# Optimization experiments

Measured on AMD Instinct MI355X. Metric: run time of the kernel, lower is better.

The kernel has to match this reference:

```python
import jax, jax.numpy as jnp
import numpy as np

D_MODEL = 1024
N_HEADS = 16
D_K = D_MODEL // N_HEADS
SEQ = 4096
BATCH = 1
THETA = 10000.0


def setup_inputs() -> dict:
    key = jax.random.key(0)
    ks = jax.random.split(key, 5)
    scale = 0.02
    x = jax.random.normal(ks[0], (BATCH, SEQ, D_MODEL), dtype=jnp.float32)
    token_positions = jnp.broadcast_to(jnp.arange(SEQ, dtype=jnp.int64 if jax.config.jax_enable_x64 else jnp.int32)[None, :], (BATCH, SEQ))
    Wq = jax.random.normal(ks[1], (D_MODEL, D_MODEL), dtype=jnp.float32) * scale
    Wk = jax.random.normal(ks[2], (D_MODEL, D_MODEL), dtype=jnp.float32) * scale
    Wv = jax.random.normal(ks[3], (D_MODEL, D_MODEL), dtype=jnp.float32) * scale
    Wo = jax.random.normal(ks[4], (D_MODEL, D_MODEL), dtype=jnp.float32) * scale
    return {"x": x, "token_positions": token_positions, "Wq": Wq, "Wk": Wk, "Wv": Wv, "Wo": Wo}


def _apply_rope(t, token_positions, theta=THETA):
    # t: (b, h, s, d_k); token_positions: (b, s)
    d_k = t.shape[-1]
    inv_freq = theta ** (-jnp.arange(0, d_k, 2, dtype=jnp.float32) / d_k)  # (d_k/2,)
    ang = token_positions.astype(jnp.float32)[:, :, None] * inv_freq  # (b, s, d_k/2)
    cos = jnp.cos(ang)[:, None, :, :]  # (b, 1, s, d_k/2)
    sin = jnp.sin(ang)[:, None, :, :]
    te, to = t[..., 0::2], t[..., 1::2]
    re = te * cos - to * sin
    ro = te * sin + to * cos
    # interleave back: (..., d_k/2, 2) -> (..., d_k)
    return jnp.stack([re, ro], axis=-1).reshape(t.shape)


def reference(x, token_positions, Wq, Wk, Wv, Wo):
    b, s, d_model = x.shape
    h, d_k = N_HEADS, D_K
    q = (x @ Wq.T).reshape(b, s, h, d_k).transpose(0, 2, 1, 3)  # (b,h,s,d_k)
    k = (x @ Wk.T).reshape(b, s, h, d_k).transpose(0, 2, 1, 3)
    v = (x @ Wv.T).reshape(b, s, h, d_k).transpose(0, 2, 1, 3)
    q = _apply_rope(q, token_positions)
    k = _apply_rope(k, token_positions)
    scores = jnp.einsum('bhqd,bhkd->bhqk', q, k) / jnp.sqrt(jnp.float32(d_k))
    causal = jnp.tril(jnp.ones((s, s), dtype=bool))[None, None]
    scores = jnp.where(causal, scores, jnp.float32(-1e9))
    attn = jax.nn.softmax(scores, axis=-1)
    out = jnp.einsum('bhqk,bhkd->bhqd', attn, v)  # (b,h,s,d_k)
    out = out.transpose(0, 2, 1, 3).reshape(b, s, d_model)
    return out @ Wo.T
```

## Files before the change

kernel.cpp:

```cpp
#include <hip/hip_runtime.h>
#include <hip/hip_bf16.h>
#include <math.h>


#define SEQ 4096
#define DM  1024
#define NH  16
#define DK  64

typedef __attribute__((ext_vector_type(8))) short short8;
typedef __attribute__((ext_vector_type(4))) float floatx4;
typedef __attribute__((ext_vector_type(4))) short short4v;

static __device__ __forceinline__ short f2bf(float f) {
    __hip_bfloat16 h = __float2bfloat16(f);
    return __builtin_bit_cast(short, h);
}

static __device__ __forceinline__ float fast_exp2(float x) {
#if __has_builtin(__builtin_amdgcn_exp2f)
    return __builtin_amdgcn_exp2f(x);
#else
    return exp2f(x);
#endif
}

static __device__ __forceinline__ short8 load8_f32_as_bf16(const float* p) {
    float4 a = *reinterpret_cast<const float4*>(p);
    float4 b = *reinterpret_cast<const float4*>(p + 4);
    short8 s;
    s[0] = f2bf(a.x); s[1] = f2bf(a.y); s[2] = f2bf(a.z); s[3] = f2bf(a.w);
    s[4] = f2bf(b.x); s[5] = f2bf(b.y); s[6] = f2bf(b.z); s[7] = f2bf(b.w);
    return s;
}

static __device__ __forceinline__ void gl2lds16(const __hip_bfloat16* g, short* l) {
    __builtin_amdgcn_global_load_lds(
        (const __attribute__((address_space(1))) unsigned int*)g,
        (__attribute__((address_space(3))) unsigned int*)l, 16, 0, 0);
}

static __device__ __forceinline__ int read_pos(const int* tp32, int s) {
    return (tp32[1] == 1) ? tp32[s] : tp32[2 * s];
}

__global__ __launch_bounds__(256) void prep_kernel(
    const float* __restrict__ x,  const float* __restrict__ Wq,
    const float* __restrict__ Wk, const float* __restrict__ Wv,
    const int* __restrict__ tp,
    __hip_bfloat16* __restrict__ xb,  __hip_bfloat16* __restrict__ Wqb,
    __hip_bfloat16* __restrict__ Wkb, __hip_bfloat16* __restrict__ Wvb,
    float2* __restrict__ tab)
{
    int b = blockIdx.x;
    if (b < 3584) {
        const float* src; __hip_bfloat16* dst; int off;
        if (b < 2048)      { src = x;  dst = xb;  off = b; }
        else if (b < 2560) { src = Wq; dst = Wqb; off = b - 2048; }
        else if (b < 3072) { src = Wk; dst = Wkb; off = b - 2560; }
        else               { src = Wv; dst = Wvb; off = b - 3072; }
        size_t i = (size_t)off * 256 + threadIdx.x;
        short8 v = load8_f32_as_bf16(src + i * 8);
        *reinterpret_cast<short8*>((short*)dst + i * 8) = v;
    } else {
        int idx = (b - 3584) * 256 + threadIdx.x;
        if (idx < SEQ * 32) {
            int s = idx >> 5, pair = idx & 31;
            float inv_freq = exp2f(-(float)(2 * pair) * (13.287712379549449f / 64.f));
            float sn, cs;
            sincosf((float)read_pos(tp, s) * inv_freq, &sn, &cs);
            tab[idx] = make_float2(cs, sn);
        }
    }
}

__global__ __launch_bounds__(256) void qkv_rope_kernel(
    const __hip_bfloat16* __restrict__ xb,
    const float2* __restrict__ tab,
    const __hip_bfloat16* __restrict__ Wqb,
    const __hip_bfloat16* __restrict__ Wkb,
    const __hip_bfloat16* __restrict__ Wvb,
    __hip_bfloat16* __restrict__ q_ws,
    __hip_bfloat16* __restrict__ k_ws,
    __hip_bfloat16* __restrict__ vt_ws)
{
    __shared__ __align__(16) short pool[17408];
    short* As = pool;
    short* Bs = pool + 8192;

    const int by = blockIdx.y;
    const int wsel = by >> 3;
    const __hip_bfloat16* W = (wsel == 0) ? Wqb : (wsel == 1 ? Wkb : Wvb);
    const int nloc0 = (by & 7) * 128;
    const int m0 = blockIdx.x * 128;

    const int t = threadIdx.x;
    const int lane = t & 63;
    const int w = t >> 6;
    const int quad = lane >> 4;
    const int ln = lane & 15;
    const int wm = (w >> 1) * 64;
    const int wn = (w & 1) * 64;

    floatx4 acc[4][4];
    #pragma unroll
    for (int i = 0; i < 4; i++)
        #pragma unroll
        for (int j = 0; j < 4; j++) acc[i][j] = (floatx4){0.f, 0.f, 0.f, 0.f};

    for (int k0 = 0; k0 < DM; k0 += 64) {
        #pragma unroll
        for (int it = 0; it < 4; it++) {
            int row = w * 32 + it * 8 + (lane >> 3);
            int sg = (lane & 7) ^ (row & 7);
            gl2lds16(&xb[(size_t)(m0 + row) * DM + k0 + sg * 8], &As[(w * 32 + it * 8) * 64]);
            gl2lds16(&W[(size_t)(nloc0 + row) * DM + k0 + sg * 8], &Bs[(w * 32 + it * 8) * 64]);
        }
        __syncthreads();

        short8 af[4][2], bfr[4][2];
        #pragma unroll
        for (int i = 0; i < 4; i++)
            #pragma unroll
            for (int kc = 0; kc < 2; kc++)
                af[i][kc] = *reinterpret_cast<const short8*>(
                    &As[(wm + i * 16 + ln) * 64 + (((kc * 4 + quad) ^ (ln & 7)) << 3)]);
        #pragma unroll
        for (int j = 0; j < 4; j++)
            #pragma unroll
            for (int kc = 0; kc < 2; kc++)
                bfr[j][kc] = *reinterpret_cast<const short8*>(
                    &Bs[(wn + j * 16 + ln) * 64 + (((kc * 4 + quad) ^ (ln & 7)) << 3)]);

        #pragma unroll
        for (int kc = 0; kc < 2; kc++)
            #pragma unroll
            for (int i = 0; i < 4; i++)
                #pragma unroll
                for (int j = 0; j < 4; j++)
                    acc[i][j] = __builtin_amdgcn_mfma_f32_16x16x32_bf16(
                        af[i][kc], bfr[j][kc], acc[i][j], 0, 0, 0);
        __syncthreads();
    }

    if (wsel < 2) {
        __hip_bfloat16* dst = (wsel == 0) ? q_ws : k_ws;
        const float qscale = (wsel == 0) ? 0.18033688011112042f : 1.0f;
        #pragma unroll
        for (int j = 0; j < 4; j++) {
            int cnl = wn + j * 16 + ln;
            int pair = ((nloc0 + cnl) & 63) >> 1;
            #pragma unroll
            for (int i = 0; i < 4; i++) {
                int rowl = wm + i * 16 + quad * 4;
                #pragma unroll
                for (int r = 0; r < 4; r++) {
                    float2 t2 = tab[(size_t)(m0 + rowl + r) * 32 + pair];
                    float val = acc[i][j][r];
                    float partner = __shfl_xor(val, 1, 64);
                    float res = val * t2.x + (((lane & 1) ? partner : -partner) * t2.y);
                    pool[(rowl + r) * 136 + cnl] = f2bf(res * qscale);
                }
            }
        }
        __syncthreads();
        int row = t >> 1, half = t & 1;
        size_t gbase = (size_t)(m0 + row) * DM + nloc0 + half * 64;
        #pragma unroll
        for (int c = 0; c < 8; c++)
            *reinterpret_cast<short8*>(&dst[gbase + c * 8]) =
                *reinterpret_cast<const short8*>(&pool[row * 136 + half * 64 + c * 8]);
    } else {
        #pragma unroll
        for (int j = 0; j < 4; j++) {
            int cnl = wn + j * 16 + ln;
            #pragma unroll
            for (int i = 0; i < 4; i++) {
                int s0 = wm + i * 16 + quad * 4;
                #pragma unroll
                for (int r = 0; r < 4; r++)
                    pool[cnl * 136 + s0 + r] = f2bf(acc[i][j][r]);
            }
        }
        __syncthreads();
        int cnl = t >> 1, sh = t & 1;
        size_t base = (size_t)(nloc0 + cnl) * SEQ + m0 + sh * 64;
        #pragma unroll
        for (int c = 0; c < 8; c++)
            *reinterpret_cast<short8*>(&vt_ws[base + c * 8]) =
                *reinterpret_cast<const short8*>(&pool[cnl * 136 + sh * 64 + c * 8]);
    }
}

__global__ __launch_bounds__(512) void attn_kernel(
    const __hip_bfloat16* __restrict__ q_ws,
    const __hip_bfloat16* __restrict__ k_ws,
    const __hip_bfloat16* __restrict__ vt_ws,
    __hip_bfloat16* __restrict__ o_ws)
{
    __shared__ __align__(16) short Kt[2][2][64 * 64];
    __shared__ __align__(16) short Vt[2][2][64 * 64];
    __shared__ __align__(16) short P[8][2][16 * 64];

    const int head = blockIdx.y;
    const int bx = blockIdx.x;
    const int qbA0 = (31 - bx) * 128;
    const int qbB0 = bx * 128;
    const int t = threadIdx.x;
    const int lane = t & 63;
    const int w = t >> 6;
    const int quad = lane >> 4;
    const int ln = lane & 15;
    const int nstep = (31 - bx) + 1;

    const int qAbase = qbA0 + w * 16;
    const int qBbase = qbB0 + w * 16;
    const int e = ((ln & 7) << 1) ^ (ln & 8);

    const int keyl = w * 8 + (lane >> 3);
    const int sg = (lane & 7) ^ (keyl & 7);

    auto stage = [&](int b, int kb) {
        #pragma unroll
        for (int h = 0; h < 2; h++) {
            gl2lds16(&k_ws[(size_t)(kb + h * 64 + keyl) * DM + head * 64 + sg * 8],
                     &Kt[b][h][w * 512]);
            gl2lds16(&vt_ws[(size_t)(head * 64 + keyl) * SEQ + kb + h * 64 + sg * 8],
                     &Vt[b][h][w * 512]);
        }
    };

    short8 qfA[2], qfB[2];
    #pragma unroll
    for (int kk = 0; kk < 2; kk++) {
        qfA[kk] = *reinterpret_cast<const short8*>(
            &q_ws[(size_t)(qAbase + ln) * DM + head * 64 + kk * 32 + quad * 8]);
        qfB[kk] = *reinterpret_cast<const short8*>(
            &q_ws[(size_t)(qBbase + ln) * DM + head * 64 + kk * 32 + quad * 8]);
    }

    floatx4 accA[4], accB[4];
    float lA = 0.f, lB = 0.f;
    #pragma unroll
    for (int nt = 0; nt < 4; nt++) {
        accA[nt] = (floatx4){0.f, 0.f, 0.f, 0.f};
        accB[nt] = (floatx4){0.f, 0.f, 0.f, 0.f};
    }
    const floatx4 zero4 = {0.f, 0.f, 0.f, 0.f};

    stage(0, 0);
    int buf = 0;
    for (int st = 0; st < nstep; st++) {
        __syncthreads();
        if (st + 1 < nstep) stage(buf ^ 1, (st + 1) * 128);

        const int kb0 = st * 128;
        const int kb1 = kb0 + 64;
        const bool aA1 = (kb1 <= qAbase + 15);
        const bool aB0 = (kb0 <= qBbase + 15);
        const bool aB1 = (kb1 <= qBbase + 15);

        short8 kf[2][4][2], vf[2][4][2];
        #pragma unroll
        for (int h = 0; h < 2; h++)
            #pragma unroll
            for (int nt = 0; nt < 4; nt++)
                #pragma unroll
                for (int kk = 0; kk < 2; kk++) {
                    const int off = (nt * 16 + ln) * 64 + (((kk * 4 + quad) ^ (ln & 7)) << 3);
                    kf[h][nt][kk] = *reinterpret_cast<const short8*>(&Kt[buf][h][off]);
                    vf[h][nt][kk] = *reinterpret_cast<const short8*>(&Vt[buf][h][off]);
                }

        auto tile = [&](const short8 (&qf)[2], floatx4 (&acc)[4], float& l,
                        const int qbase, const bool a1) {
            const int qpos = qbase + ln;
            floatx4 s[4];
            __builtin_amdgcn_s_setprio(1);
            #pragma unroll
            for (int nt = 0; nt < 4; nt++) {
                floatx4 x0 = __builtin_amdgcn_mfma_f32_16x16x32_bf16(kf[0][nt][0], qf[0], zero4, 0, 0, 0);
                s[nt] = __builtin_amdgcn_mfma_f32_16x16x32_bf16(kf[0][nt][1], qf[1], x0, 0, 0, 0);
            }
            __builtin_amdgcn_s_setprio(0);
            if (kb0 + 63 > qbase) {
                #pragma unroll
                for (int nt = 0; nt < 4; nt++) {
                    int kbase = kb0 + nt * 16 + quad * 4;
                    #pragma unroll
                    for (int r = 0; r < 4; r++)
                        if (kbase + r > qpos) s[nt][r] = -1e9f;
                }
            }
            #pragma unroll
            for (int nt = 0; nt < 4; nt++) {
                #pragma unroll
                for (int r = 0; r < 4; r++) {
                    float p = fast_exp2(s[nt][r]);
                    s[nt][r] = p;
                    l += p;
                }
                short4v pk = { f2bf(s[nt][0]), f2bf(s[nt][1]),
                               f2bf(s[nt][2]), f2bf(s[nt][3]) };
                *reinterpret_cast<short4v*>(&P[w][0][ln * 64 + (((nt * 4 + quad) ^ e) << 2)]) = pk;
            }
            if (a1) {
                __builtin_amdgcn_s_setprio(1);
                #pragma unroll
                for (int nt = 0; nt < 4; nt++) {
                    floatx4 x0 = __builtin_amdgcn_mfma_f32_16x16x32_bf16(kf[1][nt][0], qf[0], zero4, 0, 0, 0);
                    s[nt] = __builtin_amdgcn_mfma_f32_16x16x32_bf16(kf[1][nt][1], qf[1], x0, 0, 0, 0);
                }
                __builtin_amdgcn_s_setprio(0);
                if (kb1 + 63 > qbase) {
                    #pragma unroll
                    for (int nt = 0; nt < 4; nt++) {
                        int kbase = kb1 + nt * 16 + quad * 4;
                        #pragma unroll
                        for (int r = 0; r < 4; r++)
                            if (kbase + r > qpos) s[nt][r] = -1e9f;
                    }
                }
                #pragma unroll
                for (int nt = 0; nt < 4; nt++) {
                    #pragma unroll
                    for (int r = 0; r < 4; r++) {
                        float p = fast_exp2(s[nt][r]);
                        s[nt][r] = p;
                        l += p;
                    }
                    short4v pk = { f2bf(s[nt][0]), f2bf(s[nt][1]),
                                   f2bf(s[nt][2]), f2bf(s[nt][3]) };
                    *reinterpret_cast<short4v*>(&P[w][1][ln * 64 + (((nt * 4 + quad) ^ e) << 2)]) = pk;
                }
            }
            {
                short8 pa[2];
                #pragma unroll
                for (int kk = 0; kk < 2; kk++)
                    pa[kk] = *reinterpret_cast<const short8*>(
                        &P[w][0][ln * 64 + (((kk * 8 + quad * 2) ^ e) << 2)]);
                __builtin_amdgcn_s_setprio(1);
                #pragma unroll
                for (int nt = 0; nt < 4; nt++) {
                    floatx4 o = __builtin_amdgcn_mfma_f32_16x16x32_bf16(pa[0], vf[0][nt][0], acc[nt], 0, 0, 0);
                    acc[nt] = __builtin_amdgcn_mfma_f32_16x16x32_bf16(pa[1], vf[0][nt][1], o, 0, 0, 0);
                }
                __builtin_amdgcn_s_setprio(0);
            }
            if (a1) {
                short8 pa[2];
                #pragma unroll
                for (int kk = 0; kk < 2; kk++)
                    pa[kk] = *reinterpret_cast<const short8*>(
                        &P[w][1][ln * 64 + (((kk * 8 + quad * 2) ^ e) << 2)]);
                __builtin_amdgcn_s_setprio(1);
                #pragma unroll
                for (int nt = 0; nt < 4; nt++) {
                    floatx4 o = __builtin_amdgcn_mfma_f32_16x16x32_bf16(pa[0], vf[1][nt][0], acc[nt], 0, 0, 0);
                    acc[nt] = __builtin_amdgcn_mfma_f32_16x16x32_bf16(pa[1], vf[1][nt][1], o, 0, 0, 0);
                }
                __builtin_amdgcn_s_setprio(0);
            }
        };

        tile(qfA, accA, lA, qAbase, aA1);
        if (aB0) tile(qfB, accB, lB, qBbase, aB1);

        buf ^= 1;
    }

    {
        float l = lA;
        l += __shfl_xor(l, 16, 64);
        l += __shfl_xor(l, 32, 64);
        #pragma unroll
        for (int r = 0; r < 4; r++) {
            float rl = 1.f / __shfl(l, quad * 4 + r, 64);
            int row = qAbase + quad * 4 + r;
            #pragma unroll
            for (int nt = 0; nt < 4; nt++)
                o_ws[(size_t)row * DM + head * 64 + nt * 16 + ln] =
                    __float2bfloat16(accA[nt][r] * rl);
        }
    }
    {
        float l = lB;
        l += __shfl_xor(l, 16, 64);
        l += __shfl_xor(l, 32, 64);
        #pragma unroll
        for (int r = 0; r < 4; r++) {
            float rl = 1.f / __shfl(l, quad * 4 + r, 64);
            int row = qBbase + quad * 4 + r;
            #pragma unroll
            for (int nt = 0; nt < 4; nt++)
                o_ws[(size_t)row * DM + head * 64 + nt * 16 + ln] =
                    __float2bfloat16(accB[nt][r] * rl);
        }
    }
}

__global__ __launch_bounds__(256) void oproj_kernel(
    const __hip_bfloat16* __restrict__ o_in,
    const float* __restrict__ Wo,
    float* __restrict__ out)
{
    __shared__ __align__(16) char smem[24576];
    short* As = (short*)smem;
    short* Bs = As + 8192;
    float* fpool = (float*)smem;

    const int m0 = blockIdx.x * 128;
    const int n0 = blockIdx.y * 64;

    const int t = threadIdx.x;
    const int lane = t & 63;
    const int w = t >> 6;
    const int quad = lane >> 4;
    const int ln = lane & 15;
    const int wm = (w >> 1) * 64;
    const int wn = (w & 1) * 32;

    floatx4 acc[4][2];
    #pragma unroll
    for (int i = 0; i < 4; i++)
        #pragma unroll
        for (int j = 0; j < 2; j++) acc[i][j] = (floatx4){0.f, 0.f, 0.f, 0.f};

    for (int k0 = 0; k0 < DM; k0 += 64) {
        #pragma unroll
        for (int it = 0; it < 4; it++) {
            int row = w * 32 + it * 8 + (lane >> 3);
            int sg = (lane & 7) ^ (row & 7);
            gl2lds16(&o_in[(size_t)(m0 + row) * DM + k0 + sg * 8], &As[(w * 32 + it * 8) * 64]);
        }
        #pragma unroll
        for (int p = 0; p < 2; p++) {
            int r = (t >> 3) + p * 32;
            int sg2 = t & 7;
            *reinterpret_cast<short8*>(&Bs[r * 64 + ((sg2 ^ (r & 7)) << 3)]) =
                load8_f32_as_bf16(&Wo[(size_t)(n0 + r) * DM + k0 + sg2 * 8]);
        }
        __syncthreads();

        short8 af[4][2], bfr[2][2];
        #pragma unroll
        for (int i = 0; i < 4; i++)
            #pragma unroll
            for (int kc = 0; kc < 2; kc++)
                af[i][kc] = *reinterpret_cast<const short8*>(
                    &As[(wm + i * 16 + ln) * 64 + (((kc * 4 + quad) ^ (ln & 7)) << 3)]);
        #pragma unroll
        for (int j = 0; j < 2; j++)
            #pragma unroll
            for (int kc = 0; kc < 2; kc++)
                bfr[j][kc] = *reinterpret_cast<const short8*>(
                    &Bs[(wn + j * 16 + ln) * 64 + (((kc * 4 + quad) ^ (ln & 7)) << 3)]);

        #pragma unroll
        for (int kc = 0; kc < 2; kc++)
            #pragma unroll
            for (int i = 0; i < 4; i++)
                #pragma unroll
                for (int j = 0; j < 2; j++)
                    acc[i][j] = __builtin_amdgcn_mfma_f32_16x16x32_bf16(
                        af[i][kc], bfr[j][kc], acc[i][j], 0, 0, 0);
        __syncthreads();
    }

    #pragma unroll
    for (int ph = 0; ph < 2; ph++) {
        if ((w >> 1) == ph) {
            #pragma unroll
            for (int j = 0; j < 2; j++)
                #pragma unroll
                for (int i = 0; i < 4; i++) {
                    int rl = i * 16 + quad * 4;
                    #pragma unroll
                    for (int r = 0; r < 4; r++)
                        fpool[(rl + r) * 68 + wn + j * 16 + ln] = acc[i][j][r];
                }
        }
        __syncthreads();
        int row = t >> 2;
        int c0 = (t & 3) * 16;
        size_t gbase = (size_t)(m0 + ph * 64 + row) * DM + n0 + c0;
        #pragma unroll
        for (int c = 0; c < 4; c++)
            *reinterpret_cast<float4*>(&out[gbase + c * 4]) =
                *reinterpret_cast<const float4*>(&fpool[row * 68 + c0 + c * 4]);
        __syncthreads();
    }
}

extern "C" void kernel_launch(void* const* d_in, const int* in_sizes, int n_in,
                              void* d_out, int out_size, void* d_ws, size_t ws_size,
                              hipStream_t stream) {
    const float* x  = (const float*)d_in[0];
    const int* tp   = (const int*)d_in[1];
    const float* Wq = (const float*)d_in[2];
    const float* Wk = (const float*)d_in[3];
    const float* Wv = (const float*)d_in[4];
    const float* Wo = (const float*)d_in[5];
    float* out = (float*)d_out;

    char* ws = (char*)d_ws;
    const size_t MB = 1024 * 1024;
    __hip_bfloat16* xb    = (__hip_bfloat16*)(ws);
    __hip_bfloat16* q_ws  = (__hip_bfloat16*)(ws + 8  * MB);
    __hip_bfloat16* k_ws  = (__hip_bfloat16*)(ws + 16 * MB);
    __hip_bfloat16* vt_ws = (__hip_bfloat16*)(ws + 24 * MB);
    __hip_bfloat16* o_ws  = xb;
    __hip_bfloat16* Wqb = (__hip_bfloat16*)d_out;
    __hip_bfloat16* Wkb = Wqb + (size_t)DM * DM;
    __hip_bfloat16* Wvb = Wkb + (size_t)DM * DM;
    float2* tab = (float2*)((char*)d_out + 6 * MB);

    prep_kernel<<<4096, 256, 0, stream>>>(x, Wq, Wk, Wv, tp, xb, Wqb, Wkb, Wvb, tab);
    qkv_rope_kernel<<<dim3(32, 24), 256, 0, stream>>>(xb, tab, Wqb, Wkb, Wvb, q_ws, k_ws, vt_ws);
    attn_kernel<<<dim3(16, 16), 512, 0, stream>>>(q_ws, k_ws, vt_ws, o_ws);
    oproj_kernel<<<dim3(32, 16), 256, 0, stream>>>(o_ws, Wo, out);
}
```

Measured before the change: 223.1 us.

## Shrink attention blocks to 256 threads, 64-row query tiles, with XCD-aware block remap

The attention kernel now uses 4 waves per block with 64-row query tiles, paired causally as (63-bx, bx), and launches 512 blocks instead of 256. Block IDs are remapped so that consecutive work for a head lands on the same XCD. The inner loop is restructured to load K/V fragments per 64-key half, halving the fragment registers. It also interleaves QK/softmax for both tiles before the PV MMAs. The goal is better occupancy (launch_bounds 256,2), finer load balance and L2 locality. The cost is that each staged K/V tile is shared by fewer query rows.

After: 218.1 us. 1.02x faster.

```diff
diff --git a/kernel.cpp b/kernel.cpp
--- a/kernel.cpp
+++ b/kernel.cpp
@@ -192,7 +192,7 @@
     }
 }
 
-__global__ __launch_bounds__(512) void attn_kernel(
+__global__ __launch_bounds__(256, 2) void attn_kernel(
     const __hip_bfloat16* __restrict__ q_ws,
     const __hip_bfloat16* __restrict__ k_ws,
     const __hip_bfloat16* __restrict__ vt_ws,
@@ -200,34 +200,38 @@
 {
     __shared__ __align__(16) short Kt[2][2][64 * 64];
     __shared__ __align__(16) short Vt[2][2][64 * 64];
-    __shared__ __align__(16) short P[8][2][16 * 64];
-
-    const int head = blockIdx.y;
-    const int bx = blockIdx.x;
-    const int qbA0 = (31 - bx) * 128;
-    const int qbB0 = bx * 128;
+    __shared__ __align__(16) short P[4][2][16 * 64];
+
+    const int bid = (int)blockIdx.x + 32 * (int)blockIdx.y;
+    const int wg  = (bid & 7) * 64 + (bid >> 3);
+    const int head = wg >> 5;
+    const int bx   = wg & 31;
+
+    const int qbA0 = (63 - bx) * 64;
+    const int qbB0 = bx * 64;
     const int t = threadIdx.x;
     const int lane = t & 63;
     const int w = t >> 6;
     const int quad = lane >> 4;
     const int ln = lane & 15;
-    const int nstep = (31 - bx) + 1;
+    const int nstep = (qbA0 + 63) / 128 + 1;
 
     const int qAbase = qbA0 + w * 16;
     const int qBbase = qbB0 + w * 16;
     const int e = ((ln & 7) << 1) ^ (ln & 8);
 
-    const int keyl = w * 8 + (lane >> 3);
-    const int sg = (lane & 7) ^ (keyl & 7);
-
     auto stage = [&](int b, int kb) {
         #pragma unroll
-        for (int h = 0; h < 2; h++) {
-            gl2lds16(&k_ws[(size_t)(kb + h * 64 + keyl) * DM + head * 64 + sg * 8],
-                     &Kt[b][h][w * 512]);
-            gl2lds16(&vt_ws[(size_t)(head * 64 + keyl) * SEQ + kb + h * 64 + sg * 8],
-                     &Vt[b][h][w * 512]);
-        }
+        for (int h = 0; h < 2; h++)
+            #pragma unroll
+            for (int i = 0; i < 2; i++) {
+                int keyl = w * 16 + i * 8 + (lane >> 3);
+                int sg = (lane & 7) ^ (keyl & 7);
+                gl2lds16(&k_ws[(size_t)(kb + h * 64 + keyl) * DM + head * 64 + sg * 8],
+                         &Kt[b][h][(w * 16 + i * 8) * 64]);
+                gl2lds16(&vt_ws[(size_t)(head * 64 + keyl) * SEQ + kb + h * 64 + sg * 8],
+                         &Vt[b][h][(w * 16 + i * 8) * 64]);
+            }
     };
 
     short8 qfA[2], qfB[2];
@@ -254,68 +258,37 @@
         __syncthreads();
         if (st + 1 < nstep) stage(buf ^ 1, (st + 1) * 128);
 
-        const int kb0 = st * 128;
-        const int kb1 = kb0 + 64;
-        const bool aA1 = (kb1 <= qAbase + 15);
-        const bool aB0 = (kb0 <= qBbase + 15);
-        const bool aB1 = (kb1 <= qBbase + 15);
-
-        short8 kf[2][4][2], vf[2][4][2];
-        #pragma unroll
-        for (int h = 0; h < 2; h++)
+        #pragma unroll
+        for (int h = 0; h < 2; h++) {
+            const int kb = st * 128 + h * 64;
+            const bool actA = (h == 0) || (kb <= qAbase + 15);
+            const bool actB = (kb <= qBbase + 15);
+            if (!actA && !actB) continue;
+
+            short8 kf[4][2], vf[4][2];
             #pragma unroll
             for (int nt = 0; nt < 4; nt++)
                 #pragma unroll
                 for (int kk = 0; kk < 2; kk++) {
                     const int off = (nt * 16 + ln) * 64 + (((kk * 4 + quad) ^ (ln & 7)) << 3);
-                    kf[h][nt][kk] = *reinterpret_cast<const short8*>(&Kt[buf][h][off]);
-                    vf[h][nt][kk] = *reinterpret_cast<const short8*>(&Vt[buf][h][off]);
-                }
-
-        auto tile = [&](const short8 (&qf)[2], floatx4 (&acc)[4], float& l,
-                        const int qbase, const bool a1) {
-            const int qpos = qbase + ln;
-            floatx4 s[4];
-            __builtin_amdgcn_s_setprio(1);
-            #pragma unroll
-            for (int nt = 0; nt < 4; nt++) {
-                floatx4 x0 = __builtin_amdgcn_mfma_f32_16x16x32_bf16(kf[0][nt][0], qf[0], zero4, 0, 0, 0);
-                s[nt] = __builtin_amdgcn_mfma_f32_16x16x32_bf16(kf[0][nt][1], qf[1], x0, 0, 0, 0);
-            }
-            __builtin_amdgcn_s_setprio(0);
-            if (kb0 + 63 > qbase) {
+                    kf[nt][kk] = *reinterpret_cast<const short8*>(&Kt[buf][h][off]);
+                    vf[nt][kk] = *reinterpret_cast<const short8*>(&Vt[buf][h][off]);
+                }
+
+            auto qk_sm = [&](const short8 (&qf)[2], float& l, int qbase, int pslot) {
+                floatx4 s[4];
+                __builtin_amdgcn_s_setprio(1);
                 #pragma unroll
                 for (int nt = 0; nt < 4; nt++) {
-                    int kbase = kb0 + nt * 16 + quad * 4;
-                    #pragma unroll
-                    for (int r = 0; r < 4; r++)
-                        if (kbase + r > qpos) s[nt][r] = -1e9f;
-                }
-            }
-            #pragma unroll
-            for (int nt = 0; nt < 4; nt++) {
-                #pragma unroll
-                for (int r = 0; r < 4; r++) {
-                    float p = fast_exp2(s[nt][r]);
-                    s[nt][r] = p;
-                    l += p;
-                }
-                short4v pk = { f2bf(s[nt][0]), f2bf(s[nt][1]),
-                               f2bf(s[nt][2]), f2bf(s[nt][3]) };
-                *reinterpret_cast<short4v*>(&P[w][0][ln * 64 + (((nt * 4 + quad) ^ e) << 2)]) = pk;
-            }
-            if (a1) {
-                __builtin_amdgcn_s_setprio(1);
-                #pragma unroll
-                for (int nt = 0; nt < 4; nt++) {
-                    floatx4 x0 = __builtin_amdgcn_mfma_f32_16x16x32_bf16(kf[1][nt][0], qf[0], zero4, 0, 0, 0);
-                    s[nt] = __builtin_amdgcn_mfma_f32_16x16x32_bf16(kf[1][nt][1], qf[1], x0, 0, 0, 0);
+                    floatx4 x0 = __builtin_amdgcn_mfma_f32_16x16x32_bf16(kf[nt][0], qf[0], zero4, 0, 0, 0);
+                    s[nt] = __builtin_amdgcn_mfma_f32_16x16x32_bf16(kf[nt][1], qf[1], x0, 0, 0, 0);
                 }
                 __builtin_amdgcn_s_setprio(0);
-                if (kb1 + 63 > qbase) {
+                const int qpos = qbase + ln;
+                if (kb + 63 > qbase) {
                     #pragma unroll
                     for (int nt = 0; nt < 4; nt++) {
-                        int kbase = kb1 + nt * 16 + quad * 4;
+                        int kbase = kb + nt * 16 + quad * 4;
                         #pragma unroll
                         for (int r = 0; r < 4; r++)
                             if (kbase + r > qpos) s[nt][r] = -1e9f;
@@ -331,42 +304,29 @@
                     }
                     short4v pk = { f2bf(s[nt][0]), f2bf(s[nt][1]),
                                    f2bf(s[nt][2]), f2bf(s[nt][3]) };
-                    *reinterpret_cast<short4v*>(&P[w][1][ln * 64 + (((nt * 4 + quad) ^ e) << 2)]) = pk;
-                }
-            }
-            {
+                    *reinterpret_cast<short4v*>(&P[w][pslot][ln * 64 + (((nt * 4 + quad) ^ e) << 2)]) = pk;
+                }
+            };
+            auto pv = [&](floatx4 (&acc)[4], int pslot) {
                 short8 pa[2];
                 #pragma unroll
                 for (int kk = 0; kk < 2; kk++)
                     pa[kk] = *reinterpret_cast<const short8*>(
-                        &P[w][0][ln * 64 + (((kk * 8 + quad * 2) ^ e) << 2)]);
+                        &P[w][pslot][ln * 64 + (((kk * 8 + quad * 2) ^ e) << 2)]);
                 __builtin_amdgcn_s_setprio(1);
                 #pragma unroll
                 for (int nt = 0; nt < 4; nt++) {
-                    floatx4 o = __builtin_amdgcn_mfma_f32_16x16x32_bf16(pa[0], vf[0][nt][0], acc[nt], 0, 0, 0);
-                    acc[nt] = __builtin_amdgcn_mfma_f32_16x16x32_bf16(pa[1], vf[0][nt][1], o, 0, 0, 0);
+                    floatx4 o = __builtin_amdgcn_mfma_f32_16x16x32_bf16(pa[0], vf[nt][0], acc[nt], 0, 0, 0);
+                    acc[nt] = __builtin_amdgcn_mfma_f32_16x16x32_bf16(pa[1], vf[nt][1], o, 0, 0, 0);
                 }
                 __builtin_amdgcn_s_setprio(0);
-            }
-            if (a1) {
-                short8 pa[2];
-                #pragma unroll
-                for (int kk = 0; kk < 2; kk++)
-                    pa[kk] = *reinterpret_cast<const short8*>(
-                        &P[w][1][ln * 64 + (((kk * 8 + quad * 2) ^ e) << 2)]);
-                __builtin_amdgcn_s_setprio(1);
-                #pragma unroll
-                for (int nt = 0; nt < 4; nt++) {
-                    floatx4 o = __builtin_amdgcn_mfma_f32_16x16x32_bf16(pa[0], vf[1][nt][0], acc[nt], 0, 0, 0);
-                    acc[nt] = __builtin_amdgcn_mfma_f32_16x16x32_bf16(pa[1], vf[1][nt][1], o, 0, 0, 0);
-                }
-                __builtin_amdgcn_s_setprio(0);
-            }
-        };
-
-        tile(qfA, accA, lA, qAbase, aA1);
-        if (aB0) tile(qfB, accB, lB, qBbase, aB1);
-
+            };
+
+            if (actA) qk_sm(qfA, lA, qAbase, 0);
+            if (actB) qk_sm(qfB, lB, qBbase, 1);
+            if (actA) pv(accA, 0);
+            if (actB) pv(accB, 1);
+        }
         buf ^= 1;
     }
 
@@ -518,6 +478,6 @@
 
     prep_kernel<<<4096, 256, 0, stream>>>(x, Wq, Wk, Wv, tp, xb, Wqb, Wkb, Wvb, tab);
     qkv_rope_kernel<<<dim3(32, 24), 256, 0, stream>>>(xb, tab, Wqb, Wkb, Wvb, q_ws, k_ws, vt_ws);
-    attn_kernel<<<dim3(16, 16), 512, 0, stream>>>(q_ws, k_ws, vt_ws, o_ws);
+    attn_kernel<<<dim3(32, 16), 256, 0, stream>>>(q_ws, k_ws, vt_ws, o_ws);
     oproj_kernel<<<dim3(32, 16), 256, 0, stream>>>(o_ws, Wo, out);
 }
```
